# Performance work log

Measured on AMD Instinct MI355X. Metric: run time of the kernel, lower is better.

## Reference

```python
import jax, jax.numpy as jnp
import numpy as np

N, D, E, DFF = 8192, 1024, 8, 4096


def setup_inputs() -> dict:
    key = jax.random.key(0)
    k1, k2, k3, k4 = jax.random.split(key, 4)
    x = jax.random.normal(k1, (N, D), dtype=jnp.float32)
    gate_w = jax.random.normal(k2, (D, E), dtype=jnp.float32) * 0.02
    w1 = jax.random.normal(k3, (E, D, DFF), dtype=jnp.float32) * 0.02
    w2 = jax.random.normal(k4, (E, DFF, D), dtype=jnp.float32) * 0.02
    return {"x": x, "gate_w": gate_w, "w1": w1, "w2": w2, "top_k": 2}


def reference(x, gate_w, w1, w2, top_k):
    # Router: softmax over experts, top-k, renormalize top-k weights.
    gate_logits = x @ gate_w                          # [N, E]
    gate_probs = jax.nn.softmax(gate_logits, axis=-1)  # [N, E]
    top_w, top_i = jax.lax.top_k(gate_probs, top_k)    # [N, k]
    top_w = top_w / jnp.sum(top_w, axis=-1, keepdims=True)
    # Dense combine weights: zero except at the top-k experts per token.
    n = x.shape[0]
    dense_w = jnp.zeros_like(gate_probs).at[jnp.arange(n)[:, None], top_i].set(top_w)  # [N, E]
    # Per-expert SiLU MLP, weighted combine. Loop over small fixed E.
    y = jnp.zeros_like(x)
    for e in range(w1.shape[0]):
        h = jax.nn.silu(x @ w1[e]) @ w2[e]            # [N, D]
        y = y + dense_w[:, e:e + 1] * h
    return y
```

## Files before the change

kernel.cpp:

```cpp
#include <hip/hip_runtime.h>


#define N_TOK 8192
#define DIM   1024
#define NE    8
#define DFF   4096
#define BM 128
#define BN 128
#define BK 64
#define QE 4

typedef unsigned short u16;
typedef short bf16x8 __attribute__((ext_vector_type(8)));
typedef float f32x4  __attribute__((ext_vector_type(4)));

#define TOKE_OFF   0u
#define TOKW_OFF   32768u
#define TLIST_OFF  65536u
#define WLIST_OFF  131072u
#define COUNTS_OFF 196608u
#define BASEP_OFF  196672u
#define CURSOR_OFF 196736u
#define XB_OFF     1048576u
#define H_OFF      17825792u
#define WT_OFF     152043520u

__device__ __forceinline__ float bf2f(u16 h) {
    return __uint_as_float(((unsigned)h) << 16);
}
__device__ __forceinline__ u16 f2bf(float f) {
    unsigned u = __float_as_uint(f);
    unsigned r = u + 0x7FFFu + ((u >> 16) & 1u);
    return (u16)(r >> 16);
}

__global__ void convert_x(const float* __restrict__ x, u16* __restrict__ xb) {
    int idx = (blockIdx.x * 256 + threadIdx.x) * 4;
    float4 v = *(const float4*)&x[idx];
    ushort4 o;
    o.x = f2bf(v.x); o.y = f2bf(v.y); o.z = f2bf(v.z); o.w = f2bf(v.w);
    *(ushort4*)&xb[idx] = o;
}

__global__ void convtrans(const float* __restrict__ in, u16* __restrict__ out,
                          int R, int C) {
    __shared__ float tile[32][33];
    int z = blockIdx.z;
    const float* src = in  + (size_t)z * R * C;
    u16*         dst = out + (size_t)z * R * C;
    int c0 = blockIdx.x * 32, r0 = blockIdx.y * 32;
    int tx = threadIdx.x & 31, ty = threadIdx.x >> 5;
#pragma unroll
    for (int i = 0; i < 32; i += 8)
        tile[ty + i][tx] = src[(size_t)(r0 + ty + i) * C + c0 + tx];
    __syncthreads();
#pragma unroll
    for (int i = 0; i < 32; i += 8)
        dst[(size_t)(c0 + ty + i) * R + r0 + tx] = f2bf(tile[tx][ty + i]);
}

__global__ void gate_kernel(const float* __restrict__ x, const float* __restrict__ gw,
                            int* __restrict__ tok_e, float* __restrict__ tok_w,
                            int* __restrict__ counts) {
    __shared__ float gsm[NE * DIM];
    int t = blockIdx.x, lane = threadIdx.x;
    for (int i = lane; i < NE * DIM; i += 64) {
        int d = i >> 3, e = i & 7;
        gsm[e * DIM + d] = gw[i];
    }
    __syncthreads();
    float acc[NE];
#pragma unroll
    for (int e = 0; e < NE; ++e) acc[e] = 0.f;
    const float* xr = x + (size_t)t * DIM;
    for (int i = lane; i < DIM; i += 64) {
        float xv = xr[i];
#pragma unroll
        for (int e = 0; e < NE; ++e) acc[e] += xv * gsm[e * DIM + i];
    }
#pragma unroll
    for (int off = 32; off > 0; off >>= 1) {
#pragma unroll
        for (int e = 0; e < NE; ++e) acc[e] += __shfl_xor(acc[e], off, 64);
    }
    if (lane == 0) {
        int a = 0;
#pragma unroll
        for (int e = 1; e < NE; ++e) if (acc[e] > acc[a]) a = e;
        int b = (a == 0) ? 1 : 0;
#pragma unroll
        for (int e = 0; e < NE; ++e) if (e != a && acc[e] > acc[b]) b = e;
        float wa = 1.f / (1.f + __expf(acc[b] - acc[a]));
        tok_e[t] = (a << 3) | b;
        tok_w[t] = wa;
        atomicAdd(&counts[a], 1);
        atomicAdd(&counts[b], 1);
    }
}

__global__ void scan_kernel(const int* __restrict__ counts, int* __restrict__ basep,
                            int* __restrict__ cursor) {
    if (threadIdx.x == 0) {
        int s = 0;
        for (int e = 0; e < NE; ++e) { basep[e] = s; s += counts[e]; cursor[e] = 0; }
    }
}

__global__ void assign_kernel(const int* __restrict__ tok_e, const float* __restrict__ tok_w,
                              const int* __restrict__ basep, int* __restrict__ cursor,
                              int* __restrict__ tlist, float* __restrict__ wlist) {
    int t = blockIdx.x * 256 + threadIdx.x;
    if (t >= N_TOK) return;
    int ee = tok_e[t];
    int a = ee >> 3, b = ee & 7;
    float wa = tok_w[t];
    int pa = atomicAdd(&cursor[a], 1);
    int sa = basep[a] + pa;
    tlist[sa] = t;  wlist[sa] = wa;
    int pb = atomicAdd(&cursor[b], 1);
    int sb = basep[b] + pb;
    tlist[sb] = t;  wlist[sb] = 1.f - wa;
}

__global__ __launch_bounds__(256) void gemm1_silu(
        const u16* __restrict__ xb, const u16* __restrict__ w1t,
        const int* __restrict__ tlist, const int* __restrict__ counts,
        const int* __restrict__ basep, u16* __restrict__ H, int ebase) {
    int bx = blockIdx.x;
    int le = bx >> 11;
    int e  = ebase + le;
    int mt = (bx >> 5) & 63;
    int nt = bx & 31;
    int cnt = counts[e];
    int row0 = mt * BM;
    if (row0 >= cnt) return;
    int nv = cnt - row0; if (nv > BM) nv = BM;
    int gb = basep[e] + row0;

    __shared__ __align__(16) u16 As[BM * BK];
    __shared__ __align__(16) u16 Bs[BN * BK];

    int tid = threadIdx.x;
    int lane = tid & 63, wid = tid >> 6;
    int wm = (wid & 1) * 64, wn = (wid >> 1) * 64;

    int srow = tid >> 3;
    int skc  = tid & 7;
    const u16* aptr[4];
#pragma unroll
    for (int i = 0; i < 4; ++i) {
        int r = srow + i * 32;
        int rr = (r < nv) ? r : 0;
        aptr[i] = xb + (size_t)tlist[gb + rr] * DIM + skc * 8;
    }
    const u16* bptr = w1t + ((size_t)le * DFF + (size_t)nt * BN + srow) * DIM + skc * 8;

    f32x4 acc[4][4];
#pragma unroll
    for (int i = 0; i < 4; ++i)
#pragma unroll
        for (int j = 0; j < 4; ++j) acc[i][j] = (f32x4){0.f, 0.f, 0.f, 0.f};

    for (int k0 = 0; k0 < DIM; k0 += BK) {
#pragma unroll
        for (int i = 0; i < 4; ++i) {
            int r = srow + i * 32;
            *(uint4*)&As[(r * 8 + (skc ^ (r & 7))) * 8] = *(const uint4*)(aptr[i] + k0);
            *(uint4*)&Bs[(r * 8 + (skc ^ (r & 7))) * 8] =
                *(const uint4*)(bptr + (size_t)i * 32 * DIM + k0);
        }
        __syncthreads();
#pragma unroll
        for (int ks = 0; ks < 2; ++ks) {
            int kc = ks * 4 + (lane >> 4);
            bf16x8 af[4], bfr[4];
#pragma unroll
            for (int mi = 0; mi < 4; ++mi) {
                int r = wm + mi * 16 + (lane & 15);
                af[mi] = *(const bf16x8*)&As[(r * 8 + (kc ^ (r & 7))) * 8];
            }
#pragma unroll
            for (int ni = 0; ni < 4; ++ni) {
                int r = wn + ni * 16 + (lane & 15);
                bfr[ni] = *(const bf16x8*)&Bs[(r * 8 + (kc ^ (r & 7))) * 8];
            }
#pragma unroll
            for (int mi = 0; mi < 4; ++mi)
#pragma unroll
                for (int ni = 0; ni < 4; ++ni)
                    acc[mi][ni] = __builtin_amdgcn_mfma_f32_16x16x32_bf16(
                        af[mi], bfr[ni], acc[mi][ni], 0, 0, 0);
        }
        __syncthreads();
    }
#pragma unroll
    for (int mi = 0; mi < 4; ++mi) {
#pragma unroll
        for (int r = 0; r < 4; ++r) {
            int row = wm + mi * 16 + (lane >> 4) * 4 + r;
            if (row < nv) {
                size_t ho = (size_t)(gb + row) * DFF + nt * BN + wn + (lane & 15);
#pragma unroll
                for (int ni = 0; ni < 4; ++ni) {
                    float v = acc[mi][ni][r];
                    H[ho + ni * 16] = f2bf(v / (1.f + __expf(-v)));
                }
            }
        }
    }
}

__global__ __launch_bounds__(256) void gemm2_combine(
        const u16* __restrict__ H, const u16* __restrict__ w2t,
        const int* __restrict__ tlist, const float* __restrict__ wlist,
        const int* __restrict__ counts, const int* __restrict__ basep,
        float* __restrict__ y, int ebase) {
    int bx = blockIdx.x;
    int le = bx >> 9;
    int e  = ebase + le;
    int mt = (bx >> 3) & 63;
    int nt = bx & 7;
    int cnt = counts[e];
    int row0 = mt * BM;
    if (row0 >= cnt) return;
    int nv = cnt - row0; if (nv > BM) nv = BM;
    int gb = basep[e] + row0;

    __shared__ __align__(16) u16 As[BM * BK];
    __shared__ __align__(16) u16 Bs[BN * BK];

    int tid = threadIdx.x;
    int lane = tid & 63, wid = tid >> 6;
    int wm = (wid & 1) * 64, wn = (wid >> 1) * 64;

    int srow = tid >> 3;
    int skc  = tid & 7;
    const u16* aptr[4];
#pragma unroll
    for (int i = 0; i < 4; ++i) {
        int r = srow + i * 32;
        int rr = (r < nv) ? r : 0;
        aptr[i] = H + (size_t)(gb + rr) * DFF + skc * 8;
    }
    const u16* bptr = w2t + ((size_t)le * DIM + (size_t)nt * BN + srow) * DFF + skc * 8;

    f32x4 acc[4][4];
#pragma unroll
    for (int i = 0; i < 4; ++i)
#pragma unroll
        for (int j = 0; j < 4; ++j) acc[i][j] = (f32x4){0.f, 0.f, 0.f, 0.f};

    for (int k0 = 0; k0 < DFF; k0 += BK) {
#pragma unroll
        for (int i = 0; i < 4; ++i) {
            int r = srow + i * 32;
            *(uint4*)&As[(r * 8 + (skc ^ (r & 7))) * 8] = *(const uint4*)(aptr[i] + k0);
            *(uint4*)&Bs[(r * 8 + (skc ^ (r & 7))) * 8] =
                *(const uint4*)(bptr + (size_t)i * 32 * DFF + k0);
        }
        __syncthreads();
#pragma unroll
        for (int ks = 0; ks < 2; ++ks) {
            int kc = ks * 4 + (lane >> 4);
            bf16x8 af[4], bfr[4];
#pragma unroll
            for (int mi = 0; mi < 4; ++mi) {
                int r = wm + mi * 16 + (lane & 15);
                af[mi] = *(const bf16x8*)&As[(r * 8 + (kc ^ (r & 7))) * 8];
            }
#pragma unroll
            for (int ni = 0; ni < 4; ++ni) {
                int r = wn + ni * 16 + (lane & 15);
                bfr[ni] = *(const bf16x8*)&Bs[(r * 8 + (kc ^ (r & 7))) * 8];
            }
#pragma unroll
            for (int mi = 0; mi < 4; ++mi)
#pragma unroll
                for (int ni = 0; ni < 4; ++ni)
                    acc[mi][ni] = __builtin_amdgcn_mfma_f32_16x16x32_bf16(
                        af[mi], bfr[ni], acc[mi][ni], 0, 0, 0);
        }
        __syncthreads();
    }
#pragma unroll
    for (int mi = 0; mi < 4; ++mi) {
#pragma unroll
        for (int r = 0; r < 4; ++r) {
            int row = wm + mi * 16 + (lane >> 4) * 4 + r;
            if (row < nv) {
                int gslot = gb + row;
                int t = tlist[gslot];
                float w = wlist[gslot];
                size_t yo = (size_t)t * DIM + nt * BN + wn + (lane & 15);
#pragma unroll
                for (int ni = 0; ni < 4; ++ni)
                    atomicAdd(&y[yo + ni * 16], w * acc[mi][ni][r]);
            }
        }
    }
}

extern "C" void kernel_launch(void* const* d_in, const int* in_sizes, int n_in,
                              void* d_out, int out_size, void* d_ws, size_t ws_size,
                              hipStream_t stream) {
    const float* x  = (const float*)d_in[0];
    const float* gw = (const float*)d_in[1];
    const float* w1 = (const float*)d_in[2];
    const float* w2 = (const float*)d_in[3];
    float* y = (float*)d_out;

    char* ws = (char*)d_ws;
    int*   tok_e  = (int*)(ws + TOKE_OFF);
    float* tok_w  = (float*)(ws + TOKW_OFF);
    int*   tlist  = (int*)(ws + TLIST_OFF);
    float* wlist  = (float*)(ws + WLIST_OFF);
    int*   counts = (int*)(ws + COUNTS_OFF);
    int*   basep  = (int*)(ws + BASEP_OFF);
    int*   cursor = (int*)(ws + CURSOR_OFF);
    u16*   xb     = (u16*)(ws + XB_OFF);
    u16*   H      = (u16*)(ws + H_OFF);
    u16*   wt     = (u16*)(ws + WT_OFF);

    hipMemsetAsync(counts, 0, 32, stream);
    hipMemsetAsync(y, 0, (size_t)N_TOK * DIM * sizeof(float), stream);
    convert_x<<<N_TOK * DIM / 1024, 256, 0, stream>>>(x, xb);
    gate_kernel<<<N_TOK, 64, 0, stream>>>(x, gw, tok_e, tok_w, counts);
    scan_kernel<<<1, 64, 0, stream>>>(counts, basep, cursor);
    assign_kernel<<<N_TOK / 256, 256, 0, stream>>>(tok_e, tok_w, basep, cursor, tlist, wlist);
    for (int q = 0; q < NE / QE; ++q) {
        convtrans<<<dim3(DFF / 32, DIM / 32, QE), 256, 0, stream>>>(
            w1 + (size_t)q * QE * DIM * DFF, wt, DIM, DFF);
        gemm1_silu<<<QE * 64 * 32, 256, 0, stream>>>(xb, wt, tlist, counts, basep, H, q * QE);
    }
    for (int q = 0; q < NE / QE; ++q) {
        convtrans<<<dim3(DIM / 32, DFF / 32, QE), 256, 0, stream>>>(
            w2 + (size_t)q * QE * DFF * DIM, wt, DFF, DIM);
        gemm2_combine<<<QE * 64 * 8, 256, 0, stream>>>(H, wt, tlist, wlist, counts, basep,
                                                       y, q * QE);
    }
}
```

Baseline: 1.048 ms.

## Use direct global-to-LDS loads in GEMMs and fuse x conversion into gating

Both expert GEMM kernels now stage A and B tiles with global_load_lds builtins that write straight into shared memory. This skips the register round trip, and the XOR swizzle moves from the LDS address to the global column choice. Separately, the bf16 conversion of x is folded into a restructured gate kernel that handles 32 tokens per block with float4 loads and block-local histogram atomics. The gate change cuts launch count, global atomics and one read of x. The async LDS load relies on __syncthreads ordering being enough to wait for the DMA writes, and it fixes a per-wave layout of contiguous 16-byte lanes.

```diff
diff --git a/kernel.cpp b/kernel.cpp
--- a/kernel.cpp
+++ b/kernel.cpp
@@ -34,13 +34,10 @@
     return (u16)(r >> 16);
 }
 
-__global__ void convert_x(const float* __restrict__ x, u16* __restrict__ xb) {
-    int idx = (blockIdx.x * 256 + threadIdx.x) * 4;
-    float4 v = *(const float4*)&x[idx];
-    ushort4 o;
-    o.x = f2bf(v.x); o.y = f2bf(v.y); o.z = f2bf(v.z); o.w = f2bf(v.w);
-    *(ushort4*)&xb[idx] = o;
-}
+#define GLL16(g, l)                                                             \
+    __builtin_amdgcn_global_load_lds(                                           \
+        (const __attribute__((address_space(1))) unsigned int*)(g),             \
+        (__attribute__((address_space(3))) unsigned int*)(l), 16, 0, 0)
 
 __global__ void convtrans(const float* __restrict__ in, u16* __restrict__ out,
                           int R, int C) {
@@ -59,43 +56,62 @@
         dst[(size_t)(c0 + ty + i) * R + r0 + tx] = f2bf(tile[tx][ty + i]);
 }
 
-__global__ void gate_kernel(const float* __restrict__ x, const float* __restrict__ gw,
-                            int* __restrict__ tok_e, float* __restrict__ tok_w,
-                            int* __restrict__ counts) {
+__global__ __launch_bounds__(256) void gate_kernel(
+        const float* __restrict__ x, const float* __restrict__ gw,
+        u16* __restrict__ xb, int* __restrict__ tok_e, float* __restrict__ tok_w,
+        int* __restrict__ counts) {
     __shared__ float gsm[NE * DIM];
-    int t = blockIdx.x, lane = threadIdx.x;
-    for (int i = lane; i < NE * DIM; i += 64) {
+    __shared__ int hcnt[NE];
+    int tid = threadIdx.x;
+    if (tid < NE) hcnt[tid] = 0;
+    for (int i = tid; i < NE * DIM; i += 256) {
         int d = i >> 3, e = i & 7;
         gsm[e * DIM + d] = gw[i];
     }
     __syncthreads();
-    float acc[NE];
-#pragma unroll
-    for (int e = 0; e < NE; ++e) acc[e] = 0.f;
-    const float* xr = x + (size_t)t * DIM;
-    for (int i = lane; i < DIM; i += 64) {
-        float xv = xr[i];
-#pragma unroll
-        for (int e = 0; e < NE; ++e) acc[e] += xv * gsm[e * DIM + i];
-    }
-#pragma unroll
-    for (int off = 32; off > 0; off >>= 1) {
-#pragma unroll
-        for (int e = 0; e < NE; ++e) acc[e] += __shfl_xor(acc[e], off, 64);
-    }
-    if (lane == 0) {
-        int a = 0;
-#pragma unroll
-        for (int e = 1; e < NE; ++e) if (acc[e] > acc[a]) a = e;
-        int b = (a == 0) ? 1 : 0;
-#pragma unroll
-        for (int e = 0; e < NE; ++e) if (e != a && acc[e] > acc[b]) b = e;
-        float wa = 1.f / (1.f + __expf(acc[b] - acc[a]));
-        tok_e[t] = (a << 3) | b;
-        tok_w[t] = wa;
-        atomicAdd(&counts[a], 1);
-        atomicAdd(&counts[b], 1);
-    }
+    int lane = tid & 63, wid = tid >> 6;
+    int t0 = blockIdx.x * 32 + wid * 8;
+    for (int tt = 0; tt < 8; ++tt) {
+        int t = t0 + tt;
+        const float4* xr  = (const float4*)(x  + (size_t)t * DIM);
+        ushort4*      xbr = (ushort4*)(xb + (size_t)t * DIM);
+        float acc[NE];
+#pragma unroll
+        for (int e = 0; e < NE; ++e) acc[e] = 0.f;
+#pragma unroll
+        for (int j = 0; j < 4; ++j) {
+            float4 xv = xr[j * 64 + lane];
+            ushort4 o;
+            o.x = f2bf(xv.x); o.y = f2bf(xv.y); o.z = f2bf(xv.z); o.w = f2bf(xv.w);
+            xbr[j * 64 + lane] = o;
+            int dbase = (j * 64 + lane) * 4;
+#pragma unroll
+            for (int e = 0; e < NE; ++e) {
+                float4 g = *(const float4*)&gsm[e * DIM + dbase];
+                acc[e] += xv.x * g.x + xv.y * g.y + xv.z * g.z + xv.w * g.w;
+            }
+        }
+#pragma unroll
+        for (int off = 32; off > 0; off >>= 1) {
+#pragma unroll
+            for (int e = 0; e < NE; ++e) acc[e] += __shfl_xor(acc[e], off, 64);
+        }
+        if (lane == 0) {
+            int a = 0;
+#pragma unroll
+            for (int e = 1; e < NE; ++e) if (acc[e] > acc[a]) a = e;
+            int b = (a == 0) ? 1 : 0;
+#pragma unroll
+            for (int e = 0; e < NE; ++e) if (e != a && acc[e] > acc[b]) b = e;
+            float wa = 1.f / (1.f + __expf(acc[b] - acc[a]));
+            tok_e[t] = (a << 3) | b;
+            tok_w[t] = wa;
+            atomicAdd(&hcnt[a], 1);
+            atomicAdd(&hcnt[b], 1);
+        }
+    }
+    __syncthreads();
+    if (tid < NE) atomicAdd(&counts[tid], hcnt[tid]);
 }
 
 __global__ void scan_kernel(const int* __restrict__ counts, int* __restrict__ basep,
@@ -144,16 +160,17 @@
     int lane = tid & 63, wid = tid >> 6;
     int wm = (wid & 1) * 64, wn = (wid >> 1) * 64;
 
-    int srow = tid >> 3;
-    int skc  = tid & 7;
-    const u16* aptr[4];
+    const u16* ga[4]; const u16* gbp[4]; int loff[4];
 #pragma unroll
     for (int i = 0; i < 4; ++i) {
-        int r = srow + i * 32;
-        int rr = (r < nv) ? r : 0;
-        aptr[i] = xb + (size_t)tlist[gb + rr] * DIM + skc * 8;
-    }
-    const u16* bptr = w1t + ((size_t)le * DFF + (size_t)nt * BN + srow) * DIM + skc * 8;
+        int cidx = (wid * 4 + i) * 64 + lane;
+        int row = cidx >> 3;
+        int cg  = (cidx & 7) ^ (row & 7);
+        int ra  = (row < nv) ? row : 0;
+        ga[i]  = xb + (size_t)tlist[gb + ra] * DIM + cg * 8;
+        gbp[i] = w1t + ((size_t)le * DFF + (size_t)nt * BN + row) * DIM + cg * 8;
+        loff[i] = (wid * 4 + i) * 512;
+    }
 
     f32x4 acc[4][4];
 #pragma unroll
@@ -164,10 +181,8 @@
     for (int k0 = 0; k0 < DIM; k0 += BK) {
 #pragma unroll
         for (int i = 0; i < 4; ++i) {
-            int r = srow + i * 32;
-            *(uint4*)&As[(r * 8 + (skc ^ (r & 7))) * 8] = *(const uint4*)(aptr[i] + k0);
-            *(uint4*)&Bs[(r * 8 + (skc ^ (r & 7))) * 8] =
-                *(const uint4*)(bptr + (size_t)i * 32 * DIM + k0);
+            GLL16(ga[i] + k0, &As[loff[i]]);
+            GLL16(gbp[i] + k0, &Bs[loff[i]]);
         }
         __syncthreads();
 #pragma unroll
@@ -233,16 +248,17 @@
     int lane = tid & 63, wid = tid >> 6;
     int wm = (wid & 1) * 64, wn = (wid >> 1) * 64;
 
-    int srow = tid >> 3;
-    int skc  = tid & 7;
-    const u16* aptr[4];
+    const u16* ga[4]; const u16* gbp[4]; int loff[4];
 #pragma unroll
     for (int i = 0; i < 4; ++i) {
-        int r = srow + i * 32;
-        int rr = (r < nv) ? r : 0;
-        aptr[i] = H + (size_t)(gb + rr) * DFF + skc * 8;
-    }
-    const u16* bptr = w2t + ((size_t)le * DIM + (size_t)nt * BN + srow) * DFF + skc * 8;
+        int cidx = (wid * 4 + i) * 64 + lane;
+        int row = cidx >> 3;
+        int cg  = (cidx & 7) ^ (row & 7);
+        int ra  = (row < nv) ? row : 0;
+        ga[i]  = H + (size_t)(gb + ra) * DFF + cg * 8;
+        gbp[i] = w2t + ((size_t)le * DIM + (size_t)nt * BN + row) * DFF + cg * 8;
+        loff[i] = (wid * 4 + i) * 512;
+    }
 
     f32x4 acc[4][4];
 #pragma unroll
@@ -253,10 +269,8 @@
     for (int k0 = 0; k0 < DFF; k0 += BK) {
 #pragma unroll
         for (int i = 0; i < 4; ++i) {
-            int r = srow + i * 32;
-            *(uint4*)&As[(r * 8 + (skc ^ (r & 7))) * 8] = *(const uint4*)(aptr[i] + k0);
-            *(uint4*)&Bs[(r * 8 + (skc ^ (r & 7))) * 8] =
-                *(const uint4*)(bptr + (size_t)i * 32 * DFF + k0);
+            GLL16(ga[i] + k0, &As[loff[i]]);
+            GLL16(gbp[i] + k0, &Bs[loff[i]]);
         }
         __syncthreads();
 #pragma unroll
@@ -323,8 +337,7 @@
 
     hipMemsetAsync(counts, 0, 32, stream);
     hipMemsetAsync(y, 0, (size_t)N_TOK * DIM * sizeof(float), stream);
-    convert_x<<<N_TOK * DIM / 1024, 256, 0, stream>>>(x, xb);
-    gate_kernel<<<N_TOK, 64, 0, stream>>>(x, gw, tok_e, tok_w, counts);
+    gate_kernel<<<N_TOK / 32, 256, 0, stream>>>(x, gw, xb, tok_e, tok_w, counts);
     scan_kernel<<<1, 64, 0, stream>>>(counts, basep, cursor);
     assign_kernel<<<N_TOK / 256, 256, 0, stream>>>(tok_e, tok_w, basep, cursor, tlist, wlist);
     for (int q = 0; q < NE / QE; ++q) {
```

After: 989.8 us. -5.6%, faster.
